# Kernel tuning notes

Measured on AMD Instinct MI355X. Metric: run time of the kernel, lower is better.

The kernel has to match this reference:

```python
import jax, jax.numpy as jnp
import numpy as np

L = 10   # lattice side (hardcoded self.length)
K = 3    # kernel_size -> half_k = 1 wrap padding
FN = 4   # filter_num
B = 262144


def setup_inputs() -> dict:
    key = jax.random.key(0)
    k1, k2, k3, k4, k5 = jax.random.split(key, 5)
    v = jax.random.normal(k1, (B, L * L), dtype=jnp.float32)
    # torch default init scale ~ 1/sqrt(fan_in)
    conv_w = jax.random.normal(k2, (FN, 1, K, K), dtype=jnp.float32) / 3.0
    conv_b = jax.random.normal(k3, (FN,), dtype=jnp.float32) * 0.1
    deconv_w = jax.random.normal(k4, (FN, 1, 2, 2), dtype=jnp.float32) / 4.0
    deconv_b = jax.random.normal(k5, (1,), dtype=jnp.float32) * 0.1
    data = jnp.zeros((1,), dtype=jnp.int32)  # unused positional arg of log_psi
    return {"v": v, "conv_w": conv_w, "conv_b": conv_b,
            "deconv_w": deconv_w, "deconv_b": deconv_b, "data": data}


def _log_psi(v, conv_w, conv_b, deconv_w, deconv_b):
    b = v.shape[0]
    x = v.reshape(b, 1, L, L)
    # handmade_padding == periodic (wrap) pad of width half_k=1 on both spatial axes
    x = jnp.pad(x, ((0, 0), (0, 0), (1, 1), (1, 1)), mode="wrap")  # [B,1,12,12]
    # Conv2d(1, FN, 3), VALID -> [B,FN,10,10]
    y = jax.lax.conv_general_dilated(
        x, conv_w, window_strides=(1, 1), padding="VALID",
        dimension_numbers=("NCHW", "OIHW", "NCHW"))
    y = y + conv_b[None, :, None, None]
    # MaxPool2d(2,2): non-overlapping 2x2 -> [B,FN,5,5]
    y = y.reshape(b, FN, L // 2, 2, L // 2, 2).max(axis=(3, 5))
    # ConvTranspose2d(FN,1,kernel=2,stride=2): each input pixel -> disjoint 2x2 block
    # torch weight layout [in=FN, out=1, 2, 2]
    z = jnp.einsum("bcij,cokl->boikjl", y, deconv_w).reshape(b, 1, L, L)
    z = z + deconv_b[None, :, None, None]
    sign_z = jnp.sign(z)
    abs_z = z * sign_z
    sign_prod = sign_z.reshape(b, -1).prod(axis=1)        # scalar per sample
    log_sum = jnp.log(abs_z).reshape(b, -1).sum(axis=1)   # scalar per sample
    return sign_prod, log_sum


def reference(v, conv_w, conv_b, deconv_w, deconv_b, data):
    return _log_psi(v, conv_w, conv_b, deconv_w, deconv_b)
```

## Files before the change

### kernel.cpp

```cpp
#include <hip/hip_runtime.h>
#include <math.h>


typedef float v2f __attribute__((ext_vector_type(2)));

#define SREAD(x) __int_as_float(__builtin_amdgcn_readfirstlane(__float_as_int(x)))
#define WAITVM(N) asm volatile("s_waitcnt vmcnt(" #N ")" ::: "memory")

__device__ __forceinline__ float dpp_swap1_f(float x) {
    return __int_as_float(__builtin_amdgcn_mov_dpp(__float_as_int(x), 0xB1, 0xF, 0xF, true));
}
__device__ __forceinline__ float dpp_swap2_f(float x) {
    return __int_as_float(__builtin_amdgcn_mov_dpp(__float_as_int(x), 0x4E, 0xF, 0xF, true));
}
__device__ __forceinline__ unsigned dpp_swap1_u(unsigned x) {
    return (unsigned)__builtin_amdgcn_mov_dpp((int)x, 0xB1, 0xF, 0xF, true);
}
__device__ __forceinline__ unsigned dpp_swap2_u(unsigned x) {
    return (unsigned)__builtin_amdgcn_mov_dpp((int)x, 0x4E, 0xF, 0xF, true);
}

__device__ __forceinline__ void gload16(const float* g, float* l) {
    __builtin_amdgcn_global_load_lds(
        (const __attribute__((address_space(1))) void*)g,
        (__attribute__((address_space(3))) void*)l, 16, 0, 0);
}
__device__ __forceinline__ void gload4(const float* g, float* l) {
    __builtin_amdgcn_global_load_lds(
        (const __attribute__((address_space(1))) void*)g,
        (__attribute__((address_space(3))) void*)l, 4, 0, 0);
}

__global__ __launch_bounds__(128, 4) void CNN2D_37495064494620_kernel(
    const float* __restrict__ v,
    const float* __restrict__ cw,
    const float* __restrict__ cb,
    const float* __restrict__ dw,
    const float* __restrict__ db,
    float* __restrict__ out,
    int B)
{
    const int lane = threadIdx.x & 63;
    const int w    = threadIdx.x >> 6;
    const int q    = lane & 1;
    const int h    = (lane >> 1) & 1;
    const int g    = lane >> 2;

    __shared__ __align__(16) float smraw[3200];
    float* sm = smraw + w * 1600;

    const float* gb = v + (size_t)(blockIdx.x * 2 + w) * 1600;
    #pragma unroll
    for (int k = 0; k < 6; ++k)
        gload16(gb + k * 256 + lane * 4, sm + k * 256);
    gload4(gb + 1536 + lane, sm + 1536);

    float Wf[4][9];
    #pragma unroll
    for (int f = 0; f < 4; ++f)
        #pragma unroll
        for (int t = 0; t < 9; ++t)
            Wf[f][t] = SREAD(cw[f * 9 + t]);
    v2f Wsel[9];
    #pragma unroll
    for (int t = 0; t < 9; ++t)
        Wsel[t] = (v2f){ h ? Wf[2][t] : Wf[0][t], h ? Wf[3][t] : Wf[1][t] };
    const float cb0 = SREAD(cb[0]), cb1 = SREAD(cb[1]);
    const float cb2 = SREAD(cb[2]), cb3 = SREAD(cb[3]);
    const v2f Cbsel = (v2f){ h ? cb2 : cb0, h ? cb3 : cb1 };

    float Dw4[4][4];
    #pragma unroll
    for (int f = 0; f < 4; ++f)
        #pragma unroll
        for (int t = 0; t < 4; ++t)
            Dw4[f][t] = SREAD(dw[f * 4 + t]);
    const float Db = SREAD(db[0]);
    float Dkl[4];
    #pragma unroll
    for (int f = 0; f < 4; ++f) {
        const float e01 = h ? Dw4[f][1] : Dw4[f][0];
        const float e23 = h ? Dw4[f][3] : Dw4[f][2];
        Dkl[f] = q ? e23 : e01;
    }
    const float Ds0 = h ? Dkl[2] : Dkl[0];
    const float Ds1 = h ? Dkl[3] : Dkl[1];
    const float Ds2 = h ? Dkl[0] : Dkl[2];
    const float Ds3 = h ? Dkl[1] : Dkl[3];

    WAITVM(0);

    const float* my  = sm + g * 100;
    const float* myq = my + q * 10;
    const float* mx  = my + (q ? 0 : 90);

    auto load5 = [&](float* dst, const float* src) {
        #pragma unroll
        for (int t = 0; t < 5; ++t) {
            float2 x = *(const float2*)(src + 2 * t);
            dst[2 * t] = x.x; dst[2 * t + 1] = x.y;
        }
    };

    unsigned sb = 0u;
    float l2 = 0.0f;
    float zpend = 0.0f;

    float X[2][10];
    float RB[10];
    load5(X[0], mx);

    #pragma unroll
    for (int i = 0; i < 5; ++i) {
        load5(RB, myq + 20 * i);
        load5(X[(i + 1) & 1], (i == 4) ? mx : (myq + 10 + 20 * i));
        const float* R0 = X[i & 1];
        const float* R1 = RB;
        const float* R2 = X[(i + 1) & 1];

        #pragma unroll
        for (int j = 0; j < 5; ++j) {
            v2f a0 = Cbsel, a1 = Cbsel;
            #pragma unroll
            for (int kc = 0; kc < 3; ++kc) {
                const int cc0 = (2 * j + kc + 9) % 10;
                const int cc1 = (2 * j + 1 + kc + 9) % 10;
                {
                    const v2f x0 = (v2f){R0[cc0], R0[cc0]};
                    const v2f x1 = (v2f){R0[cc1], R0[cc1]};
                    a0 = __builtin_elementwise_fma(x0, Wsel[kc], a0);
                    a1 = __builtin_elementwise_fma(x1, Wsel[kc], a1);
                }
                {
                    const v2f x0 = (v2f){R1[cc0], R1[cc0]};
                    const v2f x1 = (v2f){R1[cc1], R1[cc1]};
                    a0 = __builtin_elementwise_fma(x0, Wsel[3 + kc], a0);
                    a1 = __builtin_elementwise_fma(x1, Wsel[3 + kc], a1);
                }
                {
                    const v2f x0 = (v2f){R2[cc0], R2[cc0]};
                    const v2f x1 = (v2f){R2[cc1], R2[cc1]};
                    a0 = __builtin_elementwise_fma(x0, Wsel[6 + kc], a0);
                    a1 = __builtin_elementwise_fma(x1, Wsel[6 + kc], a1);
                }
            }
            const v2f m = __builtin_elementwise_max(a0, a1);
            const float Px = fmaxf(m.x, dpp_swap1_f(m.x));
            const float Py = fmaxf(m.y, dpp_swap1_f(m.y));
            const float Qx = dpp_swap2_f(Px);
            const float Qy = dpp_swap2_f(Py);
            float z = Db;
            z = fmaf(Px, Ds0, z);
            z = fmaf(Py, Ds1, z);
            z = fmaf(Qx, Ds2, z);
            z = fmaf(Qy, Ds3, z);

            const int pos = i * 5 + j;
            if (pos == 24) {
                sb ^= __float_as_uint(z);
                l2 += __log2f(fabsf(z));
            } else if (pos & 1) {
                const float zp = zpend * z;
                sb ^= __float_as_uint(zp);
                l2 += __log2f(fabsf(zp));
            } else {
                zpend = z;
            }
        }
    }

    l2 += dpp_swap1_f(l2);
    l2 += dpp_swap2_f(l2);
    sb ^= dpp_swap1_u(sb);
    sb ^= dpp_swap2_u(sb);

    const int s = blockIdx.x * 32 + w * 16 + g;
    const int r = lane & 3;
    if (r == 0)      out[s]     = (sb & 0x80000000u) ? -1.0f : 1.0f;
    else if (r == 1) out[B + s] = l2 * 0.69314718055994531f;
}

extern "C" void kernel_launch(void* const* d_in, const int* in_sizes, int n_in,
                              void* d_out, int out_size, void* d_ws, size_t ws_size,
                              hipStream_t stream) {
    const float* v  = (const float*)d_in[0];
    const float* cw = (const float*)d_in[1];
    const float* cb = (const float*)d_in[2];
    const float* dw = (const float*)d_in[3];
    const float* db = (const float*)d_in[4];
    float* out = (float*)d_out;

    const int B = in_sizes[0] / 100;
    const int grid = B / 32;
    CNN2D_37495064494620_kernel<<<grid, 128, 0, stream>>>(v, cw, cb, dw, db, out, B);
}
```

Measured before the change: 170.9 us.

## Use single-wave blocks processing two sample groups with overlapped loads

Each block becomes a single 64-thread wave that handles 32 samples in two passes. It issues the loads for the second 16-sample chunk before computing the first chunk, so that compute on the first overlaps the second load. The row loop is no longer unrolled and reloads all three stencil rows from LDS each iteration instead of reusing rows through register rotation, trading extra LDS reads for lower register pressure. The sign and log accumulation is restructured to pair products within each row, and the launch bounds occupancy hint is removed.

```diff
diff --git a/kernel.cpp b/kernel.cpp
--- a/kernel.cpp
+++ b/kernel.cpp
@@ -6,6 +6,7 @@
 
 #define SREAD(x) __int_as_float(__builtin_amdgcn_readfirstlane(__float_as_int(x)))
 #define WAITVM(N) asm volatile("s_waitcnt vmcnt(" #N ")" ::: "memory")
+#define MEMFENCE() asm volatile("" ::: "memory")
 
 __device__ __forceinline__ float dpp_swap1_f(float x) {
     return __int_as_float(__builtin_amdgcn_mov_dpp(__float_as_int(x), 0xB1, 0xF, 0xF, true));
@@ -31,7 +32,7 @@
         (__attribute__((address_space(3))) void*)l, 4, 0, 0);
 }
 
-__global__ __launch_bounds__(128, 4) void CNN2D_37495064494620_kernel(
+__global__ __launch_bounds__(64) void CNN2D_37495064494620_kernel(
     const float* __restrict__ v,
     const float* __restrict__ cw,
     const float* __restrict__ cb,
@@ -40,20 +41,23 @@
     float* __restrict__ out,
     int B)
 {
-    const int lane = threadIdx.x & 63;
-    const int w    = threadIdx.x >> 6;
+    const int lane = threadIdx.x;
     const int q    = lane & 1;
     const int h    = (lane >> 1) & 1;
     const int g    = lane >> 2;
 
-    __shared__ __align__(16) float smraw[3200];
-    float* sm = smraw + w * 1600;
-
-    const float* gb = v + (size_t)(blockIdx.x * 2 + w) * 1600;
+    __shared__ __align__(16) float sm[3200];
+
+    const float* gbp = v + (size_t)blockIdx.x * 3200;
     #pragma unroll
     for (int k = 0; k < 6; ++k)
-        gload16(gb + k * 256 + lane * 4, sm + k * 256);
-    gload4(gb + 1536 + lane, sm + 1536);
+        gload16(gbp + k * 256 + lane * 4, sm + k * 256);
+    gload4(gbp + 1536 + lane, sm + 1536);
+    MEMFENCE();
+    #pragma unroll
+    for (int k = 0; k < 6; ++k)
+        gload16(gbp + 1600 + k * 256 + lane * 4, sm + 1600 + k * 256);
+    gload4(gbp + 3136 + lane, sm + 3136);
 
     float Wf[4][9];
     #pragma unroll
@@ -88,96 +92,99 @@
     const float Ds2 = h ? Dkl[0] : Dkl[2];
     const float Ds3 = h ? Dkl[1] : Dkl[3];
 
-    WAITVM(0);
-
-    const float* my  = sm + g * 100;
-    const float* myq = my + q * 10;
-    const float* mx  = my + (q ? 0 : 90);
-
-    auto load5 = [&](float* dst, const float* src) {
-        #pragma unroll
-        for (int t = 0; t < 5; ++t) {
-            float2 x = *(const float2*)(src + 2 * t);
-            dst[2 * t] = x.x; dst[2 * t + 1] = x.y;
-        }
-    };
-
-    unsigned sb = 0u;
-    float l2 = 0.0f;
-    float zpend = 0.0f;
-
-    float X[2][10];
-    float RB[10];
-    load5(X[0], mx);
-
-    #pragma unroll
-    for (int i = 0; i < 5; ++i) {
-        load5(RB, myq + 20 * i);
-        load5(X[(i + 1) & 1], (i == 4) ? mx : (myq + 10 + 20 * i));
-        const float* R0 = X[i & 1];
-        const float* R1 = RB;
-        const float* R2 = X[(i + 1) & 1];
-
-        #pragma unroll
-        for (int j = 0; j < 5; ++j) {
-            v2f a0 = Cbsel, a1 = Cbsel;
-            #pragma unroll
-            for (int kc = 0; kc < 3; ++kc) {
-                const int cc0 = (2 * j + kc + 9) % 10;
-                const int cc1 = (2 * j + 1 + kc + 9) % 10;
-                {
-                    const v2f x0 = (v2f){R0[cc0], R0[cc0]};
-                    const v2f x1 = (v2f){R0[cc1], R0[cc1]};
-                    a0 = __builtin_elementwise_fma(x0, Wsel[kc], a0);
-                    a1 = __builtin_elementwise_fma(x1, Wsel[kc], a1);
-                }
-                {
-                    const v2f x0 = (v2f){R1[cc0], R1[cc0]};
-                    const v2f x1 = (v2f){R1[cc1], R1[cc1]};
-                    a0 = __builtin_elementwise_fma(x0, Wsel[3 + kc], a0);
-                    a1 = __builtin_elementwise_fma(x1, Wsel[3 + kc], a1);
-                }
-                {
-                    const v2f x0 = (v2f){R2[cc0], R2[cc0]};
-                    const v2f x1 = (v2f){R2[cc1], R2[cc1]};
-                    a0 = __builtin_elementwise_fma(x0, Wsel[6 + kc], a0);
-                    a1 = __builtin_elementwise_fma(x1, Wsel[6 + kc], a1);
+    #pragma unroll 1
+    for (int b = 0; b < 2; ++b) {
+        if (b == 0) { WAITVM(7); }
+        else        { WAITVM(0); }
+
+        const float* my = sm + b * 1600 + g * 100;
+        unsigned sb = 0u;
+        float l2 = 0.0f;
+
+        #pragma unroll 1
+        for (int i = 0; i < 5; ++i) {
+            const int r1 = 2 * i + q;
+            int r0 = 2 * i - 1 + q;
+            if (i == 0 && q == 0) r0 = 9;
+            int r2 = 2 * i + 1 + q;
+            if (i == 4 && q == 1) r2 = 0;
+
+            float R0[10], R1[10], R2[10];
+            {
+                const float* p0 = my + r0 * 10;
+                const float* p1 = my + r1 * 10;
+                const float* p2 = my + r2 * 10;
+                #pragma unroll
+                for (int t = 0; t < 5; ++t) {
+                    float2 x0 = *(const float2*)(p0 + 2 * t);
+                    float2 x1 = *(const float2*)(p1 + 2 * t);
+                    float2 x2 = *(const float2*)(p2 + 2 * t);
+                    R0[2 * t] = x0.x; R0[2 * t + 1] = x0.y;
+                    R1[2 * t] = x1.x; R1[2 * t + 1] = x1.y;
+                    R2[2 * t] = x2.x; R2[2 * t + 1] = x2.y;
                 }
             }
-            const v2f m = __builtin_elementwise_max(a0, a1);
-            const float Px = fmaxf(m.x, dpp_swap1_f(m.x));
-            const float Py = fmaxf(m.y, dpp_swap1_f(m.y));
-            const float Qx = dpp_swap2_f(Px);
-            const float Qy = dpp_swap2_f(Py);
-            float z = Db;
-            z = fmaf(Px, Ds0, z);
-            z = fmaf(Py, Ds1, z);
-            z = fmaf(Qx, Ds2, z);
-            z = fmaf(Qy, Ds3, z);
-
-            const int pos = i * 5 + j;
-            if (pos == 24) {
-                sb ^= __float_as_uint(z);
-                l2 += __log2f(fabsf(z));
-            } else if (pos & 1) {
-                const float zp = zpend * z;
-                sb ^= __float_as_uint(zp);
-                l2 += __log2f(fabsf(zp));
-            } else {
-                zpend = z;
+
+            float zj[5];
+            #pragma unroll
+            for (int j = 0; j < 5; ++j) {
+                v2f a0 = Cbsel, a1 = Cbsel;
+                #pragma unroll
+                for (int kc = 0; kc < 3; ++kc) {
+                    const int cc0 = (2 * j + kc + 9) % 10;
+                    const int cc1 = (2 * j + 1 + kc + 9) % 10;
+                    {
+                        const v2f x0 = (v2f){R0[cc0], R0[cc0]};
+                        const v2f x1 = (v2f){R0[cc1], R0[cc1]};
+                        a0 = __builtin_elementwise_fma(x0, Wsel[kc], a0);
+                        a1 = __builtin_elementwise_fma(x1, Wsel[kc], a1);
+                    }
+                    {
+                        const v2f x0 = (v2f){R1[cc0], R1[cc0]};
+                        const v2f x1 = (v2f){R1[cc1], R1[cc1]};
+                        a0 = __builtin_elementwise_fma(x0, Wsel[3 + kc], a0);
+                        a1 = __builtin_elementwise_fma(x1, Wsel[3 + kc], a1);
+                    }
+                    {
+                        const v2f x0 = (v2f){R2[cc0], R2[cc0]};
+                        const v2f x1 = (v2f){R2[cc1], R2[cc1]};
+                        a0 = __builtin_elementwise_fma(x0, Wsel[6 + kc], a0);
+                        a1 = __builtin_elementwise_fma(x1, Wsel[6 + kc], a1);
+                    }
+                }
+                const v2f m = __builtin_elementwise_max(a0, a1);
+                const float Px = fmaxf(m.x, dpp_swap1_f(m.x));
+                const float Py = fmaxf(m.y, dpp_swap1_f(m.y));
+                const float Qx = dpp_swap2_f(Px);
+                const float Qy = dpp_swap2_f(Py);
+                float z = Db;
+                z = fmaf(Px, Ds0, z);
+                z = fmaf(Py, Ds1, z);
+                z = fmaf(Qx, Ds2, z);
+                z = fmaf(Qy, Ds3, z);
+                zj[j] = z;
             }
+
+            const float p01 = zj[0] * zj[1];
+            const float p23 = zj[2] * zj[3];
+            sb ^= __float_as_uint(p01);
+            sb ^= __float_as_uint(p23);
+            sb ^= __float_as_uint(zj[4]);
+            l2 += __log2f(fabsf(p01));
+            l2 += __log2f(fabsf(p23));
+            l2 += __log2f(fabsf(zj[4]));
         }
+
+        l2 += dpp_swap1_f(l2);
+        l2 += dpp_swap2_f(l2);
+        sb ^= dpp_swap1_u(sb);
+        sb ^= dpp_swap2_u(sb);
+
+        const int s = blockIdx.x * 32 + b * 16 + g;
+        const int r = lane & 3;
+        if (r == 0)      out[s]     = (sb & 0x80000000u) ? -1.0f : 1.0f;
+        else if (r == 1) out[B + s] = l2 * 0.69314718055994531f;
     }
-
-    l2 += dpp_swap1_f(l2);
-    l2 += dpp_swap2_f(l2);
-    sb ^= dpp_swap1_u(sb);
-    sb ^= dpp_swap2_u(sb);
-
-    const int s = blockIdx.x * 32 + w * 16 + g;
-    const int r = lane & 3;
-    if (r == 0)      out[s]     = (sb & 0x80000000u) ? -1.0f : 1.0f;
-    else if (r == 1) out[B + s] = l2 * 0.69314718055994531f;
 }
 
 extern "C" void kernel_launch(void* const* d_in, const int* in_sizes, int n_in,
@@ -192,5 +199,5 @@
 
     const int B = in_sizes[0] / 100;
     const int grid = B / 32;
-    CNN2D_37495064494620_kernel<<<grid, 128, 0, stream>>>(v, cw, cb, dw, db, out, B);
-}
+    CNN2D_37495064494620_kernel<<<grid, 64, 0, stream>>>(v, cw, cb, dw, db, out, B);
+}
```

After: 170.5 us. Within noise of the previous version (-0.2%).
